# Kernel tuning notes

Measured on AMD Instinct MI355X. Metric: run time of the kernel, lower is better.

Reference implementation:

```python
import jax, jax.numpy as jnp
import numpy as np

U, I, D = 2048, 4096, 64


def setup_inputs() -> dict:
    key = jax.random.key(0)
    ks = jax.random.split(key, 16)
    s = 0.02  # weight scale (xavier-ish)
    inp = {
        "ui_input_mp": jax.random.uniform(ks[0], (U, I), jnp.float32),
        "ui_input_pmp": jax.random.uniform(ks[1], (U, I), jnp.float32),
        "Wu_mp": jax.random.normal(ks[2], (D, I), jnp.float32) * s,
        "Wu_pmp": jax.random.normal(ks[3], (D, I), jnp.float32) * s,
        "Wi_mp": jax.random.normal(ks[4], (D, U), jnp.float32) * s,
        "Wi_pmp": jax.random.normal(ks[5], (D, U), jnp.float32) * s,
        "mw_mp": jax.random.normal(ks[6], (I, D), jnp.float32) * s,
        "mb_mp": jnp.zeros((I,), jnp.float32),
        "aw_mp": jax.random.normal(ks[7], (I, I), jnp.float32) * s,
        "ab_mp": jnp.zeros((I,), jnp.float32),
        "Wat_mp": jax.random.normal(ks[8], (U, U + I), jnp.float32) * s,
        "mw_pmp": jax.random.normal(ks[9], (I, D), jnp.float32) * s,
        "mb_pmp": jnp.zeros((I,), jnp.float32),
        "aw_pmp": jax.random.normal(ks[10], (I, I), jnp.float32) * s,
        "ab_pmp": jnp.zeros((I,), jnp.float32),
        "Wat_pmp": jax.random.normal(ks[11], (U, U + I), jnp.float32) * s,
        "mlp_w": jax.random.normal(ks[12], (D, 2 * D), jnp.float32) * s,
        "mlp_b": jnp.zeros((D,), jnp.float32),
        "tr_w": jax.random.normal(ks[13], (D, D), jnp.float32) * s,
        "tr_b": jnp.zeros((D,), jnp.float32),
    }
    return inp


def _attention_weights(x, mw, mb, aw, ab, Wat):
    # x: [U+I, D]; mlp Linear(D,I)+ReLU (dropout=0), then tanh
    h = jnp.tanh(jax.nn.relu(x @ mw.T + mb))          # [U+I, I]
    a = jnp.tanh(h @ aw.T + ab)                        # [U+I, I]
    scores = Wat @ a                                   # [U, I]
    return jax.nn.softmax(scores, axis=1)


def _branch(ui, Wu, Wi, mw, mb, aw, ab, Wat):
    ue = ui @ Wu.T                                     # [U, D] user embeds
    ie = ui.T @ Wi.T                                   # [I, D] item embeds
    x = jnp.concatenate([ue, ie], axis=0)              # [U+I, D]
    at = _attention_weights(x, mw, mb, aw, ab, Wat)    # [U, I]
    ue_at = at @ ie                                    # [U, D]
    return ue, ie, ue_at


def reference(ui_input_mp, ui_input_pmp, Wu_mp, Wu_pmp, Wi_mp, Wi_pmp,
              mw_mp, mb_mp, aw_mp, ab_mp, Wat_mp,
              mw_pmp, mb_pmp, aw_pmp, ab_pmp, Wat_pmp,
              mlp_w, mlp_b, tr_w, tr_b):
    mlp = lambda z: jax.nn.sigmoid(z @ mlp_w.T + mlp_b)

    ue_mp, ie_mp, ue_mp_at = _branch(ui_input_mp, Wu_mp, Wi_mp,
                                     mw_mp, mb_mp, aw_mp, ab_mp, Wat_mp)
    ue_pmp, ie_pmp, ue_pmp_at = _branch(ui_input_pmp, Wu_pmp, Wi_pmp,
                                        mw_pmp, mb_pmp, aw_pmp, ab_pmp, Wat_pmp)

    u_mp = mlp(jnp.concatenate([ue_mp, ue_mp_at], axis=1))      # [U, D]
    u_pmp = mlp(jnp.concatenate([ue_pmp, ue_pmp_at], axis=1))   # [U, D]

    rate = jax.nn.sigmoid(u_mp + u_pmp)
    user_fusion = rate * u_mp + (1.0 - rate) * u_pmp            # [U, D]

    item_embeddings = mlp(jnp.concatenate([ie_mp, ie_pmp], axis=1))  # [I, D]

    user_embeds = jnp.tanh(user_fusion @ tr_w.T + tr_b)          # [U, D]
    return user_embeds, item_embeddings
```

## Files before the change

kernel.cpp:

```cpp
#include <hip/hip_runtime.h>
#include <stdint.h>
#include <math.h>


typedef short short8 __attribute__((ext_vector_type(8)));
typedef unsigned short ushort8 __attribute__((ext_vector_type(8)));
typedef unsigned char uchar8 __attribute__((ext_vector_type(8)));
typedef float f32x4 __attribute__((ext_vector_type(4)));
typedef int int4v __attribute__((ext_vector_type(4)));
typedef int int8v __attribute__((ext_vector_type(8)));

#define DEVI static __device__ __forceinline__

DEVI unsigned short f2bf(float f) {
  uint32_t u = __builtin_bit_cast(uint32_t, f);
  return (unsigned short)((u + 0x7fffu + ((u >> 16) & 1u)) >> 16);
}
DEVI unsigned char f2fp8(float f) {
  uint32_t u = __builtin_bit_cast(uint32_t, f);
  uint32_t s = (u >> 24) & 0x80u;
  uint32_t a = u & 0x7fffffffu;
  if (a >= 0x43e00000u) return (unsigned char)(s | 0x7eu);
  if (a < 0x3c800000u) {
    float af = __builtin_bit_cast(float, a);
    uint32_t n = (uint32_t)__builtin_rintf(af * 512.0f);
    return (unsigned char)(s | n);
  }
  uint32_t r = a + 0xfffffu + ((a >> 20) & 1u);
  return (unsigned char)(s | ((r >> 20) - 960u));
}
DEVI float sigmoidf_(float x) { return 1.0f / (1.0f + expf(-x)); }

DEVI void gld16(const void* g, void* l) {
  __builtin_amdgcn_global_load_lds(
      (const __attribute__((address_space(1))) unsigned int*)g,
      (__attribute__((address_space(3))) unsigned int*)l, 16, 0, 0);
}

#define MFMA16B(a, b, c) __builtin_amdgcn_mfma_f32_16x16x32_bf16(a, b, c, 0, 0, 0)
#define MFMAMX(a, b, c)                                              \
  __builtin_amdgcn_mfma_scale_f32_16x16x128_f8f6f4(                  \
      a, b, c, 0, 0, 0, 0x7f7f7f7fu, 0, 0x7f7f7f7fu)

__global__ __launch_bounds__(256) void k_f32_to_bf16(
    const float* __restrict__ s, unsigned short* __restrict__ d, long n) {
  long i0 = ((long)blockIdx.x * 256 + threadIdx.x) * 8;
  long stride = (long)gridDim.x * 256 * 8;
  for (long i = i0; i < n; i += stride) {
    f32x4 a = *(const f32x4*)(s + i);
    f32x4 b = *(const f32x4*)(s + i + 4);
    ushort8 o;
    o[0] = f2bf(a[0]); o[1] = f2bf(a[1]); o[2] = f2bf(a[2]); o[3] = f2bf(a[3]);
    o[4] = f2bf(b[0]); o[5] = f2bf(b[1]); o[6] = f2bf(b[2]); o[7] = f2bf(b[3]);
    *(ushort8*)(d + i) = o;
  }
}

__global__ __launch_bounds__(256) void k_f32_to_fp8(
    const float* __restrict__ s, unsigned char* __restrict__ d, long n,
    float scale) {
  long i0 = ((long)blockIdx.x * 256 + threadIdx.x) * 8;
  long stride = (long)gridDim.x * 256 * 8;
  for (long i = i0; i < n; i += stride) {
    f32x4 a = *(const f32x4*)(s + i);
    f32x4 b = *(const f32x4*)(s + i + 4);
    uchar8 o;
    o[0] = f2fp8(a[0] * scale); o[1] = f2fp8(a[1] * scale);
    o[2] = f2fp8(a[2] * scale); o[3] = f2fp8(a[3] * scale);
    o[4] = f2fp8(b[0] * scale); o[5] = f2fp8(b[1] * scale);
    o[6] = f2fp8(b[2] * scale); o[7] = f2fp8(b[3] * scale);
    *(uchar8*)(d + i) = o;
  }
}

struct I4Pair { int4v lo, hi; };

template <int EPI>
__global__ __launch_bounds__(512, 4) void k_gemmMX(
    const unsigned char* __restrict__ A0, const unsigned char* __restrict__ A1,
    const unsigned char* __restrict__ B0, const unsigned char* __restrict__ B1,
    float* __restrict__ outF, unsigned char* __restrict__ oB0,
    unsigned char* __restrict__ oB1, const float* __restrict__ bias0,
    const float* __restrict__ bias1, int M, int N, int K, long zsf,
    float dsc) {
  const int gx = gridDim.x;
  const int nwg = gx * gridDim.y;
  const int flat = blockIdx.y * gx + blockIdx.x;
  const int swz = (flat & 7) * (nwg >> 3) + (flat >> 3);
  const int bxi = swz % gx, byi = swz / gx;

  const int bz = blockIdx.z;
  const unsigned char* A = bz ? A1 : A0;
  const unsigned char* B = bz ? B1 : B0;
  unsigned char* outB = bz ? oB1 : oB0;
  const float* bias = bz ? bias1 : bias0;

  __shared__ unsigned char lds[49152];
  const int tid = threadIdx.x, lane = tid & 63;
  const int wid = tid >> 6, wr = wid >> 1, wc = wid & 1;
  const int bm = bxi * 256, bn = byi * 128;
  const int rl = lane & 15, q = lane >> 4;

  const int x7 = rl & 7;
  const int c0 = ((2 * q) ^ x7) << 4;
  const int c1 = ((2 * q + 1) ^ x7) << 4;

  const unsigned char* gA = A + (size_t)bm * K;
  const unsigned char* gB = B + (size_t)bn * K;

  auto stage = [&](int kc) {
#pragma unroll
    for (int i = 0; i < 4; i++) {
      const int cid = tid + 512 * i;
      const int r = cid >> 3;
      const int go = r * K + (((cid & 7) ^ (r & 7)) << 4) + kc;
      gld16(gA + go, &lds[cid << 4]);
    }
#pragma unroll
    for (int i = 4; i < 6; i++) {
      const int cid = tid + 512 * i;
      const int r = (cid - 2048) >> 3;
      const int go = r * K + (((cid & 7) ^ (r & 7)) << 4) + kc;
      gld16(gB + go, &lds[cid << 4]);
    }
  };

  f32x4 acc[4][4] = {};

  auto frag = [&](const unsigned char* p) {
    I4Pair t;
    t.lo = *(const int4v*)(p + c0);
    t.hi = *(const int4v*)(p + c1);
    return __builtin_bit_cast(int8v, t);
  };

  for (int k0 = 0; k0 < K; k0 += 128) {
    stage(k0);
    asm volatile("s_waitcnt vmcnt(0)\ns_barrier" ::: "memory");

    int8v bf[4];
#pragma unroll
    for (int nf = 0; nf < 4; nf++)
      bf[nf] = frag(lds + 32768 + (wc * 64 + nf * 16 + rl) * 128);

    __builtin_amdgcn_s_setprio(1);
#pragma unroll
    for (int mi = 0; mi < 4; mi++) {
      int8v a = frag(lds + (wr * 64 + mi * 16 + rl) * 128);
#pragma unroll
      for (int nf = 0; nf < 4; nf++)
        acc[mi][nf] = MFMAMX(a, bf[nf], acc[mi][nf]);
    }
    __builtin_amdgcn_s_setprio(0);

    if (k0 + 128 < K) {
      asm volatile("s_barrier" ::: "memory");
    }
  }

#pragma unroll
  for (int m = 0; m < 4; m++) {
#pragma unroll
    for (int nf = 0; nf < 4; nf++) {
      const int col = bn + wc * 64 + nf * 16 + rl;
#pragma unroll
      for (int r = 0; r < 4; r++) {
        const int row = bm + wr * 64 + m * 16 + q * 4 + r;
        const float v = acc[m][nf][r] * dsc;
        if (EPI == 0)
          outF[(long)bz * zsf + (size_t)row * N + col] = v;
        else
          outB[(size_t)row * N + col] = f2fp8(tanhf(v + bias[row]));
      }
    }
  }
}

__global__ __launch_bounds__(256) void k_gemmH(
    const unsigned short* __restrict__ A0, const unsigned short* __restrict__ A1,
    const unsigned short* __restrict__ B0, const unsigned short* __restrict__ B1,
    unsigned char* __restrict__ o0, unsigned char* __restrict__ o1,
    const float* __restrict__ bias0, const float* __restrict__ bias1, int M,
    int N, int K) {
  const int bz = blockIdx.z;
  const unsigned short* A = bz ? A1 : A0;
  const unsigned short* B = bz ? B1 : B0;
  unsigned char* out8 = bz ? o1 : o0;
  const float* bias = bz ? bias1 : bias0;

  __shared__ unsigned short As[128 * 32];
  __shared__ unsigned short Bs[128 * 32];
  const int tid = threadIdx.x, lane = tid & 63, wid = tid >> 6;
  const int wr = wid >> 1, wc = wid & 1;
  const int bm = blockIdx.x * 128, bn = blockIdx.y * 128;
  const int c0 = tid, c1 = tid + 256;
  const int s0 = ((c0 & 3) ^ ((c0 >> 3) & 3)) << 3;
  const int s1 = ((c1 & 3) ^ ((c1 >> 3) & 3)) << 3;
  const int rl = lane & 15, q = lane >> 4;
  const int qe = (q ^ ((rl >> 1) & 3)) << 3;

  f32x4 acc[4][4] = {};

  for (int k0 = 0; k0 < K; k0 += 32) {
    gld16(A + (size_t)(bm + (c0 >> 2)) * K + k0 + s0, As + c0 * 8);
    gld16(A + (size_t)(bm + (c1 >> 2)) * K + k0 + s1, As + c1 * 8);
    gld16(B + (size_t)(bn + (c0 >> 2)) * K + k0 + s0, Bs + c0 * 8);
    gld16(B + (size_t)(bn + (c1 >> 2)) * K + k0 + s1, Bs + c1 * 8);
    __syncthreads();

    short8 af[4], bfr[4];
#pragma unroll
    for (int mi = 0; mi < 4; mi++)
      af[mi] = *(const short8*)(As + (wr * 64 + mi * 16 + rl) * 32 + qe);
#pragma unroll
    for (int ni = 0; ni < 4; ni++)
      bfr[ni] = *(const short8*)(Bs + (wc * 64 + ni * 16 + rl) * 32 + qe);
#pragma unroll
    for (int mi = 0; mi < 4; mi++)
#pragma unroll
      for (int ni = 0; ni < 4; ni++)
        acc[mi][ni] = MFMA16B(af[mi], bfr[ni], acc[mi][ni]);
    __syncthreads();
  }

#pragma unroll
  for (int mi = 0; mi < 4; mi++) {
#pragma unroll
    for (int ni = 0; ni < 4; ni++) {
      const int col = bn + wc * 64 + ni * 16 + rl;
#pragma unroll
      for (int r = 0; r < 4; r++) {
        const int row = bm + wr * 64 + mi * 16 + q * 4 + r;
        out8[(size_t)row * N + col] =
            f2fp8(tanhf(fmaxf(acc[mi][ni][r] + bias[col], 0.0f)));
      }
    }
  }
}

template <int AMODE, int BMODE>
__global__ __launch_bounds__(256) void k_sgemm64s(
    const void* __restrict__ A0, const void* __restrict__ A1,
    const void* __restrict__ B0, const void* __restrict__ B1,
    float* __restrict__ P, int kchunk, int lda, int ldb, int M) {
  const int br = blockIdx.z, kz = blockIdx.y, KS = gridDim.y;
  const void* Av = br ? A1 : A0;
  const void* Bv = br ? B1 : B0;

  __shared__ unsigned short As[64 * 40];
  __shared__ unsigned short Bs[64 * 40];
  const int tid = threadIdx.x, lane = tid & 63, w = tid >> 6;
  const int tm = blockIdx.x * 64;

  f32x4 acc[4] = {};
  const int kbeg = kz * kchunk, kend = kbeg + kchunk;

  for (int k0 = kbeg; k0 < kend; k0 += 32) {
    if (AMODE == 0) {
      const float* Af = (const float*)Av;
      const int m = tid >> 2, k8 = (tid & 3) << 3;
      f32x4 x0 = *(const f32x4*)(Af + (size_t)(tm + m) * lda + k0 + k8);
      f32x4 x1 = *(const f32x4*)(Af + (size_t)(tm + m) * lda + k0 + k8 + 4);
      ushort8 o;
      o[0] = f2bf(x0[0]); o[1] = f2bf(x0[1]); o[2] = f2bf(x0[2]); o[3] = f2bf(x0[3]);
      o[4] = f2bf(x1[0]); o[5] = f2bf(x1[1]); o[6] = f2bf(x1[2]); o[7] = f2bf(x1[3]);
      *(ushort8*)(As + m * 40 + k8) = o;
    } else if (AMODE == 1) {
      const float* Af = (const float*)Av;
#pragma unroll
      for (int t = 0; t < 2; t++) {
        const int c = tid + t * 256;
        const int u = c >> 4, i4 = (c & 15) << 2;
        f32x4 x = *(const f32x4*)(Af + (size_t)(k0 + u) * lda + tm + i4);
        As[(i4 + 0) * 40 + u] = f2bf(x[0]);
        As[(i4 + 1) * 40 + u] = f2bf(x[1]);
        As[(i4 + 2) * 40 + u] = f2bf(x[2]);
        As[(i4 + 3) * 40 + u] = f2bf(x[3]);
      }
    } else {
      const unsigned short* Ab = (const unsigned short*)Av;
      const int m = tid >> 2, k8 = (tid & 3) << 3;
      *(ushort8*)(As + m * 40 + k8) =
          *(const ushort8*)(Ab + (size_t)(tm + m) * lda + k0 + k8);
    }
    if (BMODE == 0) {
      const float* Bf = (const float*)Bv;
      const int n = tid >> 2, k8 = (tid & 3) << 3;
      f32x4 x0 = *(const f32x4*)(Bf + (size_t)n * ldb + k0 + k8);
      f32x4 x1 = *(const f32x4*)(Bf + (size_t)n * ldb + k0 + k8 + 4);
      ushort8 o;
      o[0] = f2bf(x0[0]); o[1] = f2bf(x0[1]); o[2] = f2bf(x0[2]); o[3] = f2bf(x0[3]);
      o[4] = f2bf(x1[0]); o[5] = f2bf(x1[1]); o[6] = f2bf(x1[2]); o[7] = f2bf(x1[3]);
      *(ushort8*)(Bs + n * 40 + k8) = o;
    } else {
      const unsigned short* Bb = (const unsigned short*)Bv;
      const int n = tid >> 2, k8 = (tid & 3) << 3;
      *(ushort8*)(Bs + n * 40 + k8) =
          *(const ushort8*)(Bb + (size_t)n * ldb + k0 + k8);
    }
    __syncthreads();

    const int kr = (lane >> 4) << 3;
    short8 a = *(const short8*)(As + (w * 16 + (lane & 15)) * 40 + kr);
#pragma unroll
    for (int ni = 0; ni < 4; ni++) {
      short8 bb = *(const short8*)(Bs + (ni * 16 + (lane & 15)) * 40 + kr);
      acc[ni] = MFMA16B(a, bb, acc[ni]);
    }
    __syncthreads();
  }

  float* out = P + ((size_t)(br * KS + kz) * M) * 64;
#pragma unroll
  for (int ni = 0; ni < 4; ni++) {
    const int col = ni * 16 + (lane & 15);
#pragma unroll
    for (int r = 0; r < 4; r++) {
      const int row = tm + w * 16 + ((lane >> 4) << 2) + r;
      out[(size_t)row * 64 + col] = acc[ni][r];
    }
  }
}

template <int WF, int WB, int WT>
__global__ __launch_bounds__(256) void k_reduce(
    const float* __restrict__ P, size_t pbr_stride, float* F0, float* F1,
    unsigned short* Bo0, unsigned short* Bo1, unsigned short* T0,
    unsigned short* T1, int M, int KS, int ldT) {
  const int br = blockIdx.y;
  const float* Pp = P + (size_t)br * pbr_stride;
  const size_t i = (size_t)blockIdx.x * 256 + threadIdx.x;
  const size_t n = (size_t)M * 64;
  float s = 0.f;
  for (int k = 0; k < KS; k++) s += Pp[(size_t)k * n + i];
  if (WF) (br ? F1 : F0)[i] = s;
  if (WB) (br ? Bo1 : Bo0)[i] = f2bf(s);
  if (WT) {
    const int row = (int)(i >> 6), col = (int)(i & 63);
    (br ? T1 : T0)[(size_t)col * ldT + row] = f2bf(s);
  }
}

__global__ __launch_bounds__(256) void k_softmax(
    const float* __restrict__ S, unsigned short* __restrict__ P0,
    unsigned short* __restrict__ P1, long slab) {
  const int row = blockIdx.x, br = blockIdx.y, tid = threadIdx.x;
  const float* s = S + (size_t)br * slab + (size_t)row * 4096;
  float v[16];
  float m = -1e30f;
#pragma unroll
  for (int j = 0; j < 16; j++) {
    v[j] = s[tid + j * 256];
    m = fmaxf(m, v[j]);
  }
  __shared__ float red[4], red2[4];
  for (int o = 32; o; o >>= 1) m = fmaxf(m, __shfl_down(m, o));
  if ((tid & 63) == 0) red[tid >> 6] = m;
  __syncthreads();
  m = fmaxf(fmaxf(red[0], red[1]), fmaxf(red[2], red[3]));
  float sum = 0.0f;
#pragma unroll
  for (int j = 0; j < 16; j++) {
    v[j] = expf(v[j] - m);
    sum += v[j];
  }
  for (int o = 32; o; o >>= 1) sum += __shfl_down(sum, o);
  if ((tid & 63) == 0) red2[tid >> 6] = sum;
  __syncthreads();
  const float inv = 1.0f / (red2[0] + red2[1] + red2[2] + red2[3]);
  unsigned short* p = (br ? P1 : P0) + (size_t)row * 4096;
#pragma unroll
  for (int j = 0; j < 16; j++) p[tid + j * 256] = f2bf(v[j] * inv);
}

__global__ __launch_bounds__(256) void k_user(
    const float* __restrict__ ue_mp, const float* __restrict__ ueat_mp,
    const float* __restrict__ ue_pmp, const float* __restrict__ ueat_pmp,
    const float* __restrict__ mlp_w, const float* __restrict__ mlp_b,
    const float* __restrict__ tr_w, const float* __restrict__ tr_b,
    float* __restrict__ out) {
  const int tid = threadIdx.x, d = tid & 63, w = tid >> 6;
  const int m = blockIdx.x * 4 + w;
  __shared__ float fus[4][64];
  float a1 = mlp_b[d], a2 = a1;
  const float* r1 = ue_mp + (size_t)m * 64;
  const float* r2 = ueat_mp + (size_t)m * 64;
  const float* r3 = ue_pmp + (size_t)m * 64;
  const float* r4 = ueat_pmp + (size_t)m * 64;
  const float* w1 = mlp_w + (size_t)d * 128;
#pragma unroll 8
  for (int k = 0; k < 64; k++) {
    const float wv = w1[k];
    a1 += r1[k] * wv;
    a2 += r3[k] * wv;
  }
#pragma unroll 8
  for (int k = 0; k < 64; k++) {
    const float wv = w1[64 + k];
    a1 += r2[k] * wv;
    a2 += r4[k] * wv;
  }
  const float u1 = sigmoidf_(a1), u2 = sigmoidf_(a2);
  const float rate = sigmoidf_(u1 + u2);
  fus[w][d] = rate * u1 + (1.0f - rate) * u2;
  __syncthreads();
  float o = tr_b[d];
  const float* tw = tr_w + (size_t)d * 64;
#pragma unroll 8
  for (int k = 0; k < 64; k++) o += fus[w][k] * tw[k];
  out[(size_t)m * 64 + d] = tanhf(o);
}

__global__ __launch_bounds__(256) void k_item(
    const float* __restrict__ ie_mp, const float* __restrict__ ie_pmp,
    const float* __restrict__ mlp_w, const float* __restrict__ mlp_b,
    float* __restrict__ out) {
  const int tid = threadIdx.x, d = tid & 63, w = tid >> 6;
  const int i = blockIdx.x * 4 + w;
  float a = mlp_b[d];
  const float* r1 = ie_mp + (size_t)i * 64;
  const float* r2 = ie_pmp + (size_t)i * 64;
  const float* wp = mlp_w + (size_t)d * 128;
#pragma unroll 8
  for (int k = 0; k < 64; k++) {
    a += r1[k] * wp[k];
    a += r2[k] * wp[64 + k];
  }
  out[(size_t)i * 64 + d] = sigmoidf_(a);
}

extern "C" void kernel_launch(void* const* d_in, const int* in_sizes, int n_in,
                              void* d_out, int out_size, void* d_ws,
                              size_t ws_size, hipStream_t stream) {
  const int U = 2048, I = 4096, D = 64, UI = 6144;
  const float WSC = 16.0f, DSC = 1.0f / 16.0f;

  const float* ui[2] = {(const float*)d_in[0], (const float*)d_in[1]};
  const float* Wu[2] = {(const float*)d_in[2], (const float*)d_in[3]};
  const float* Wi[2] = {(const float*)d_in[4], (const float*)d_in[5]};
  const float* mw[2] = {(const float*)d_in[6], (const float*)d_in[11]};
  const float* mb[2] = {(const float*)d_in[7], (const float*)d_in[12]};
  const float* aw[2] = {(const float*)d_in[8], (const float*)d_in[13]};
  const float* ab[2] = {(const float*)d_in[9], (const float*)d_in[14]};
  const float* Wat[2] = {(const float*)d_in[10], (const float*)d_in[15]};
  const float* mlp_w = (const float*)d_in[16];
  const float* mlp_b = (const float*)d_in[17];
  const float* tr_w = (const float*)d_in[18];
  const float* tr_b = (const float*)d_in[19];

  char* ws = (char*)d_ws;
  size_t off = 0;
  auto alloc = [&](size_t bytes) {
    void* p = ws + off;
    off += (bytes + 255) & ~(size_t)255;
    return p;
  };
  unsigned char* aw_f8[2] = {(unsigned char*)alloc((size_t)I * I),
                             (unsigned char*)alloc((size_t)I * I)};
  unsigned short* mw_bf[2] = {(unsigned short*)alloc((size_t)I * D * 2),
                              (unsigned short*)alloc((size_t)I * D * 2)};
  unsigned char* h_f8[2] = {(unsigned char*)alloc((size_t)UI * I),
                            (unsigned char*)alloc((size_t)UI * I)};
  unsigned char* aT_f8[2] = {(unsigned char*)alloc((size_t)I * UI),
                             (unsigned char*)alloc((size_t)I * UI)};
  float* scores = (float*)alloc((size_t)U * I * 4 * 2);
  unsigned short* at_bf[2] = {(unsigned short*)alloc((size_t)U * I * 2),
                              (unsigned short*)alloc((size_t)U * I * 2)};
  unsigned short* x_bf[2];
  float* ue_f[2];
  float* ie_f[2];
  unsigned short* ieT[2];
  float* ueat_f[2];
  for (int b = 0; b < 2; b++) {
    x_bf[b] = (unsigned short*)alloc((size_t)UI * D * 2);
    ue_f[b] = (float*)alloc((size_t)U * D * 4);
    ie_f[b] = (float*)alloc((size_t)I * D * 4);
    ieT[b] = (unsigned short*)alloc((size_t)D * I * 2);
    ueat_f[b] = (float*)alloc((size_t)U * D * 4);
  }
  float* pue = (float*)h_f8[0];
  float* pie = (float*)aT_f8[0];
  float* pueat = scores;
  unsigned char* Wat_f8[2] = {(unsigned char*)at_bf[0],
                              (unsigned char*)at_bf[1]};
  const long zsf = (long)U * I;

  const dim3 blk(256);

  k_sgemm64s<0, 0><<<dim3(U / 64, 8, 2), blk, 0, stream>>>(
      ui[0], ui[1], Wu[0], Wu[1], pue, I / 8, I, I, U);
  k_reduce<1, 1, 0><<<dim3(U * 64 / 256, 2), blk, 0, stream>>>(
      pue, (size_t)8 * U * 64, ue_f[0], ue_f[1], x_bf[0], x_bf[1], nullptr,
      nullptr, U, 8, 0);
  k_sgemm64s<1, 0><<<dim3(I / 64, 8, 2), blk, 0, stream>>>(
      ui[0], ui[1], Wi[0], Wi[1], pie, U / 8, I, U, I);
  k_reduce<1, 1, 1><<<dim3(I * 64 / 256, 2), blk, 0, stream>>>(
      pie, (size_t)8 * I * 64, ie_f[0], ie_f[1], x_bf[0] + (size_t)U * D,
      x_bf[1] + (size_t)U * D, ieT[0], ieT[1], I, 8, I);

  for (int b = 0; b < 2; b++) {
    k_f32_to_fp8<<<2048, blk, 0, stream>>>(aw[b], aw_f8[b], (long)I * I, WSC);
    k_f32_to_fp8<<<2048, blk, 0, stream>>>(Wat[b], Wat_f8[b], (long)U * UI, WSC);
    k_f32_to_bf16<<<128, blk, 0, stream>>>(mw[b], mw_bf[b], (long)I * D);
  }

  k_gemmH<<<dim3(UI / 128, I / 128, 2), blk, 0, stream>>>(
      x_bf[0], x_bf[1], mw_bf[0], mw_bf[1], h_f8[0], h_f8[1], mb[0], mb[1],
      UI, I, D);

  k_gemmMX<1><<<dim3(I / 256, UI / 128, 2), dim3(512), 0, stream>>>(
      aw_f8[0], aw_f8[1], h_f8[0], h_f8[1], nullptr, aT_f8[0], aT_f8[1],
      ab[0], ab[1], I, UI, I, 0, DSC);

  k_gemmMX<0><<<dim3(U / 256, I / 128, 2), dim3(512), 0, stream>>>(
      Wat_f8[0], Wat_f8[1], aT_f8[0], aT_f8[1], scores, nullptr, nullptr,
      nullptr, nullptr, U, I, UI, zsf, DSC);

  k_softmax<<<dim3(U, 2), blk, 0, stream>>>(scores, at_bf[0], at_bf[1], zsf);

  k_sgemm64s<2, 2><<<dim3(U / 64, 8, 2), blk, 0, stream>>>(
      at_bf[0], at_bf[1], ieT[0], ieT[1], pueat, I / 8, I, I, U);
  k_reduce<1, 0, 0><<<dim3(U * 64 / 256, 2), blk, 0, stream>>>(
      pueat, (size_t)8 * U * 64, ueat_f[0], ueat_f[1], nullptr, nullptr,
      nullptr, nullptr, U, 8, 0);

  float* out_user = (float*)d_out;
  float* out_item = (float*)d_out + (size_t)U * D;
  k_user<<<U / 4, blk, 0, stream>>>(ue_f[0], ueat_f[0], ue_f[1], ueat_f[1],
                                    mlp_w, mlp_b, tr_w, tr_b, out_user);
  k_item<<<I / 4, blk, 0, stream>>>(ie_f[0], ie_f[1], mlp_w, mlp_b, out_item);
}
```

Before: 575.7 us.

## Double-buffer FP8 GEMM LDS tiles and switch to 32x32x64 scaled MFMA

Rewrites the FP8 MX GEMM main loop to use two 64-wide K stages in LDS, so the next tile loads while the current one is computed, with a single barrier per stage. It also replaces the 16x16x128 scaled MFMA with the 32x32x64 variant, changing the fragment layout, the XOR swizzle and the epilogue row mapping. The aim is to hide global-to-LDS latency and cut LDS fragment reads per MFMA. The cost is more barriers per K and different accumulator register pressure. The loop assumes K is a multiple of 128.

```diff
diff --git a/kernel.cpp b/kernel.cpp
--- a/kernel.cpp
+++ b/kernel.cpp
@@ -7,6 +7,7 @@
 typedef unsigned short ushort8 __attribute__((ext_vector_type(8)));
 typedef unsigned char uchar8 __attribute__((ext_vector_type(8)));
 typedef float f32x4 __attribute__((ext_vector_type(4)));
+typedef float f32x16 __attribute__((ext_vector_type(16)));
 typedef int int4v __attribute__((ext_vector_type(4)));
 typedef int int8v __attribute__((ext_vector_type(8)));
 
@@ -38,8 +39,8 @@
 }
 
 #define MFMA16B(a, b, c) __builtin_amdgcn_mfma_f32_16x16x32_bf16(a, b, c, 0, 0, 0)
-#define MFMAMX(a, b, c)                                              \
-  __builtin_amdgcn_mfma_scale_f32_16x16x128_f8f6f4(                  \
+#define MFMAMX32(a, b, c)                                            \
+  __builtin_amdgcn_mfma_scale_f32_32x32x64_f8f6f4(                   \
       a, b, c, 0, 0, 0, 0x7f7f7f7fu, 0, 0x7f7f7f7fu)
 
 __global__ __launch_bounds__(256) void k_f32_to_bf16(
@@ -99,33 +100,32 @@
   const int tid = threadIdx.x, lane = tid & 63;
   const int wid = tid >> 6, wr = wid >> 1, wc = wid & 1;
   const int bm = bxi * 256, bn = byi * 128;
-  const int rl = lane & 15, q = lane >> 4;
-
-  const int x7 = rl & 7;
-  const int c0 = ((2 * q) ^ x7) << 4;
-  const int c1 = ((2 * q + 1) ^ x7) << 4;
+  const int r32 = lane & 31, hi = lane >> 5;
+
+  const int X = (r32 >> 1) & 3;
+  const int c0 = ((2 * hi) ^ X) << 4;
+  const int c1 = ((2 * hi + 1) ^ X) << 4;
 
   const unsigned char* gA = A + (size_t)bm * K;
   const unsigned char* gB = B + (size_t)bn * K;
 
-  auto stage = [&](int kc) {
-#pragma unroll
-    for (int i = 0; i < 4; i++) {
+  auto stage = [&](int kc, int bufb) {
+#pragma unroll
+    for (int i = 0; i < 2; i++) {
       const int cid = tid + 512 * i;
-      const int r = cid >> 3;
-      const int go = r * K + (((cid & 7) ^ (r & 7)) << 4) + kc;
-      gld16(gA + go, &lds[cid << 4]);
-    }
-#pragma unroll
-    for (int i = 4; i < 6; i++) {
-      const int cid = tid + 512 * i;
-      const int r = (cid - 2048) >> 3;
-      const int go = r * K + (((cid & 7) ^ (r & 7)) << 4) + kc;
-      gld16(gB + go, &lds[cid << 4]);
+      const int r = cid >> 2;
+      const int go = r * K + (((cid & 3) ^ ((cid >> 3) & 3)) << 4) + kc;
+      gld16(gA + go, &lds[bufb + (cid << 4)]);
+    }
+    {
+      const int cid = tid;
+      const int r = cid >> 2;
+      const int go = r * K + (((cid & 3) ^ ((cid >> 3) & 3)) << 4) + kc;
+      gld16(gB + go, &lds[bufb + 16384 + (cid << 4)]);
     }
   };
 
-  f32x4 acc[4][4] = {};
+  f32x16 acc[2][2] = {};
 
   auto frag = [&](const unsigned char* p) {
     I4Pair t;
@@ -134,39 +134,47 @@
     return __builtin_bit_cast(int8v, t);
   };
 
+  auto body = [&](int kc, int cb, int pb) {
+    if (kc + 64 < K) stage(kc + 64, pb);
+
+    int8v bf[2];
+#pragma unroll
+    for (int nf = 0; nf < 2; nf++)
+      bf[nf] = frag(lds + cb + 16384 + (wc * 64 + nf * 32 + r32) * 64);
+
+    __builtin_amdgcn_s_setprio(1);
+#pragma unroll
+    for (int mi = 0; mi < 2; mi++) {
+      int8v a = frag(lds + cb + (wr * 64 + mi * 32 + r32) * 64);
+#pragma unroll
+      for (int nf = 0; nf < 2; nf++)
+        acc[mi][nf] = MFMAMX32(a, bf[nf], acc[mi][nf]);
+    }
+    __builtin_amdgcn_s_setprio(0);
+
+    if (kc + 64 < K) {
+      asm volatile("s_waitcnt vmcnt(0)\ns_barrier" ::: "memory");
+    }
+  };
+
+  stage(0, 0);
+  asm volatile("s_waitcnt vmcnt(0)\ns_barrier" ::: "memory");
+
   for (int k0 = 0; k0 < K; k0 += 128) {
-    stage(k0);
-    asm volatile("s_waitcnt vmcnt(0)\ns_barrier" ::: "memory");
-
-    int8v bf[4];
-#pragma unroll
-    for (int nf = 0; nf < 4; nf++)
-      bf[nf] = frag(lds + 32768 + (wc * 64 + nf * 16 + rl) * 128);
-
-    __builtin_amdgcn_s_setprio(1);
-#pragma unroll
-    for (int mi = 0; mi < 4; mi++) {
-      int8v a = frag(lds + (wr * 64 + mi * 16 + rl) * 128);
-#pragma unroll
-      for (int nf = 0; nf < 4; nf++)
-        acc[mi][nf] = MFMAMX(a, bf[nf], acc[mi][nf]);
-    }
-    __builtin_amdgcn_s_setprio(0);
-
-    if (k0 + 128 < K) {
-      asm volatile("s_barrier" ::: "memory");
-    }
-  }
-
-#pragma unroll
-  for (int m = 0; m < 4; m++) {
-#pragma unroll
-    for (int nf = 0; nf < 4; nf++) {
-      const int col = bn + wc * 64 + nf * 16 + rl;
-#pragma unroll
-      for (int r = 0; r < 4; r++) {
-        const int row = bm + wr * 64 + m * 16 + q * 4 + r;
-        const float v = acc[m][nf][r] * dsc;
+    body(k0, 0, 24576);
+    body(k0 + 64, 24576, 0);
+  }
+
+#pragma unroll
+  for (int mi = 0; mi < 2; mi++) {
+#pragma unroll
+    for (int nf = 0; nf < 2; nf++) {
+      const int col = bn + wc * 64 + nf * 32 + r32;
+#pragma unroll
+      for (int r = 0; r < 16; r++) {
+        const int row =
+            bm + wr * 64 + mi * 32 + (r & 3) + 8 * (r >> 2) + 4 * hi;
+        const float v = acc[mi][nf][r] * dsc;
         if (EPI == 0)
           outF[(long)bz * zsf + (size_t)row * N + col] = v;
         else
```

New measurement: 578.7 us. Within noise of the previous version (+0.5%).
